# Kernel optimization log

Measured on AMD Instinct MI355X. Metric: run time of the kernel, lower is better.

## Reference

```python
import jax, jax.numpy as jnp
import numpy as np

B, S, D = 2, 11253, 256
NHEAD, NLEVEL, DFF = 8, 4, 1024
KERNEL = 2
NPOINT = KERNEL * KERNEL
HEAD_DIM = D // NHEAD
LEVEL_SHAPES = [(92, 92), (46, 46), (23, 23), (12, 12)]
LEVEL_STARTS = np.cumsum([0] + [h * w for h, w in LEVEL_SHAPES])[:-1]


def _kernel_indices():
    # BoxeR _create_kernel_indices: even kernel -> [-0.5, 0.5]/K, (x, y) order
    idx = np.arange(KERNEL, dtype=np.float32) - (KERNEL - 1) / 2.0
    i, j = np.meshgrid(idx, idx, indexing="ij")
    return jnp.asarray(np.stack([j, i], -1).reshape(-1, 2) / KERNEL)


KIDX = _kernel_indices()  # (NPOINT, 2) box-relative sample offsets


def layer_norm(x, w, b, eps=1e-5):
    mu = x.mean(-1, keepdims=True)
    var = ((x - mu) ** 2).mean(-1, keepdims=True)
    return (x - mu) * jax.lax.rsqrt(var + eps) * w + b


def setup_inputs() -> dict:
    key = jax.random.key(0)
    ks = jax.random.split(key, 12)

    def p(i, shape, scale=0.02):
        return jax.random.normal(ks[i], shape, jnp.float32) * scale

    cxcy = jax.random.uniform(ks[2], (B, S, 2), jnp.float32, minval=0.1, maxval=0.9)
    wh = jax.random.uniform(ks[3], (B, S, 2), jnp.float32, minval=0.02, maxval=0.2)
    return dict(
        src=jax.random.normal(ks[0], (B, S, D), jnp.float32),
        pos=jax.random.normal(ks[1], (B, S, D), jnp.float32),
        src_shape=jnp.asarray(np.array(LEVEL_SHAPES, np.int32)),
        src_mask=jnp.zeros((B, S), jnp.bool_),
        src_start_index=jnp.asarray(LEVEL_STARTS.astype(np.int32)),
        src_valid_ratios=jnp.ones((B, NLEVEL, 2), jnp.float32),
        ref_windows=jnp.concatenate([cxcy, wh], -1),
        value_w=p(4, (D, D)), value_b=jnp.zeros((D,), jnp.float32),
        out_w=p(5, (D, D)), out_b=jnp.zeros((D,), jnp.float32),
        box_w=p(6, (NHEAD * NLEVEL * 4, D)), box_b=jnp.zeros((NHEAD * NLEVEL * 4,), jnp.float32),
        attn_w=p(7, (NHEAD * NLEVEL * NPOINT, D)), attn_b=jnp.zeros((NHEAD * NLEVEL * NPOINT,), jnp.float32),
        lin1_w=p(8, (DFF, D)), lin1_b=jnp.zeros((DFF,), jnp.float32),
        lin2_w=p(9, (D, DFF)), lin2_b=jnp.zeros((D,), jnp.float32),
        norm1_w=jnp.ones((D,), jnp.float32), norm1_b=jnp.zeros((D,), jnp.float32),
        norm2_w=jnp.ones((D,), jnp.float32), norm2_b=jnp.zeros((D,), jnp.float32),
    )


def box_attention(q, src, src_mask, src_valid_ratios, ref_windows,
                  value_w, value_b, out_w, out_b, box_w, box_b, attn_w, attn_b):
    value = src @ value_w.T + value_b
    value = jnp.where(src_mask[..., None], 0.0, value)
    value = value.reshape(B, S, NHEAD, HEAD_DIM)

    # where-to-attend: per-head, per-level box offsets decoded around ref_windows (cx,cy,w,h)
    off = (q @ box_w.T + box_b).reshape(B, S, NHEAD, NLEVEL, 4)
    ref = ref_windows[:, :, None, None, :]
    boxes = ref + off / 8.0 * ref[..., jnp.array([2, 3, 2, 3])]
    center, size = boxes[..., None, :2], boxes[..., None, 2:]
    grid = center + KIDX * jax.nn.relu(size)  # (B,S,nh,L,P,2) in normalized [0,1] coords
    grid = grid * src_valid_ratios[:, None, None, :, None, :]

    attn = (q @ attn_w.T + attn_b).reshape(B, S, NHEAD, NLEVEL * NPOINT)
    attn = jax.nn.softmax(attn, -1).reshape(B, S, NHEAD, NLEVEL, NPOINT)

    out = jnp.zeros((B, NHEAD, S, HEAD_DIM), src.dtype)
    for lvl, (H, W) in enumerate(LEVEL_SHAPES):
        s0 = int(LEVEL_STARTS[lvl])
        v = jnp.transpose(value[:, s0:s0 + H * W], (0, 2, 1, 3))  # (B,nh,HW,hd)
        loc = jnp.transpose(grid[:, :, :, lvl], (0, 2, 1, 3, 4))  # (B,nh,S,P,2)
        # grid_sample bilinear, align_corners=False, zero padding
        px = loc[..., 0] * W - 0.5
        py = loc[..., 1] * H - 0.5
        x0, y0 = jnp.floor(px), jnp.floor(py)
        wx, wy = (px - x0)[..., None], (py - y0)[..., None]

        def gather(ix, iy):
            valid = (ix >= 0) & (ix < W) & (iy >= 0) & (iy < H)
            idx = (jnp.clip(iy, 0, H - 1) * W + jnp.clip(ix, 0, W - 1)).astype(jnp.int32)
            g = jnp.take_along_axis(v, idx.reshape(B, NHEAD, S * NPOINT)[..., None], axis=2)
            return g.reshape(B, NHEAD, S, NPOINT, HEAD_DIM) * valid[..., None]

        g00, g01 = gather(x0, y0), gather(x0 + 1, y0)
        g10, g11 = gather(x0, y0 + 1), gather(x0 + 1, y0 + 1)
        samp = (g00 * (1 - wx) + g01 * wx) * (1 - wy) + (g10 * (1 - wx) + g11 * wx) * wy
        aw = jnp.transpose(attn[:, :, :, lvl], (0, 2, 1, 3))  # (B,nh,S,P)
        out = out + jnp.einsum("bhspd,bhsp->bhsd", samp, aw)

    out = jnp.transpose(out, (0, 2, 1, 3)).reshape(B, S, D)
    return out @ out_w.T + out_b


def reference(src, pos, src_shape, src_mask, src_start_index, src_valid_ratios,
              ref_windows, value_w, value_b, out_w, out_b, box_w, box_b,
              attn_w, attn_b, lin1_w, lin1_b, lin2_w, lin2_b,
              norm1_w, norm1_b, norm2_w, norm2_b):
    # self-attn (box attention) + residual + LN
    src2 = box_attention(src + pos, src, src_mask, src_valid_ratios, ref_windows,
                         value_w, value_b, out_w, out_b, box_w, box_b, attn_w, attn_b)
    x = layer_norm(src + src2, norm1_w, norm1_b)
    # FFN + residual + LN (dropout=0 in eval)
    ff = jax.nn.relu(x @ lin1_w.T + lin1_b) @ lin2_w.T + lin2_b
    return layer_norm(x + ff, norm2_w, norm2_b)
```

## Files before the change

### kernel.cpp

```cpp
#include <hip/hip_runtime.h>
#include <hip/hip_bf16.h>
#include <hip/hip_fp16.h>

#define TOKENS 22506
#define SLEN   11253

typedef __bf16 bf16x8 __attribute__((ext_vector_type(8)));
typedef float  f32x4  __attribute__((ext_vector_type(4)));
typedef float  f32x2  __attribute__((ext_vector_type(2)));
typedef uint   u32x4  __attribute__((ext_vector_type(4)));

__device__ __forceinline__ ushort f2bu(float f) {
    __hip_bfloat16 h = __float2bfloat16(f);
    return *reinterpret_cast<ushort*>(&h);
}
__device__ __forceinline__ float bu2f(ushort u) {
    return __uint_as_float((uint)u << 16);
}
__device__ __forceinline__ uint pkf16(float a, float b) {
    __half2 h = __floats2half2_rn(a, b);
    return *reinterpret_cast<uint*>(&h);
}
__device__ __forceinline__ void gl16(const ushort* g, ushort* l) {
    __builtin_amdgcn_global_load_lds(
        (__attribute__((address_space(1))) void*)(g),
        (__attribute__((address_space(3))) void*)(l), 16, 0, 0);
}

template<bool RELU, bool NTSTORE>
__global__ __launch_bounds__(256) void gemm_small(
    const ushort* __restrict__ A0, const ushort* __restrict__ W0,
    const float* __restrict__ b0, ushort* __restrict__ C0,
    const ushort* __restrict__ A1, const ushort* __restrict__ W1,
    const float* __restrict__ b1, ushort* __restrict__ C1,
    int M, int N, int K)
{
    const bool zz = blockIdx.z != 0;
    const ushort* A   = zz ? A1 : A0;
    const ushort* W   = zz ? W1 : W0;
    const float* bias = zz ? b1 : b0;
    ushort* Cptr      = zz ? C1 : C0;

    __shared__ ushort smem[12288];
    const int tid  = threadIdx.x;
    const int lane = tid & 63;
    const int wid  = tid >> 6;
    const int wr = wid >> 1, wc = wid & 1;
    const int m0 = blockIdx.x * 64, n0 = blockIdx.y * 128;
    const int lrow = lane & 15, lhi = lane >> 4;

    const int arow = tid >> 2;
    const int scol = (tid & 3) << 3;
    const ushort* ga  = A + (size_t)min(m0 + arow, M - 1) * K + scol;
    const ushort* gb0 = W + (size_t)(n0 + arow)      * K + scol;
    const ushort* gb1 = W + (size_t)(n0 + arow + 64) * K + scol;

    f32x4 acc[2][4] = {};
    const int NT = K >> 5;

    gl16(ga,  &smem[tid * 8]);
    gl16(gb0, &smem[4096 + tid * 8]);
    gl16(gb1, &smem[4096 + tid * 8 + 2048]);

    int cur = 0;
    for (int t = 0; t < NT; ++t) {
        __syncthreads();
        if (t + 1 < NT) {
            const int k0 = (t + 1) << 5;
            const int nb = cur ^ 1;
            gl16(ga  + k0, &smem[nb * 2048 + tid * 8]);
            gl16(gb0 + k0, &smem[4096 + nb * 4096 + tid * 8]);
            gl16(gb1 + k0, &smem[4096 + nb * 4096 + tid * 8 + 2048]);
        }
        bf16x8 afr[2], bfr[4];
        #pragma unroll
        for (int m = 0; m < 2; ++m)
            afr[m] = *reinterpret_cast<const bf16x8*>(
                &smem[cur * 2048 + (wr * 32 + m * 16 + lrow) * 32 + lhi * 8]);
        #pragma unroll
        for (int n = 0; n < 4; ++n)
            bfr[n] = *reinterpret_cast<const bf16x8*>(
                &smem[4096 + cur * 4096 + (wc * 64 + n * 16 + lrow) * 32 + lhi * 8]);
        #pragma unroll
        for (int m = 0; m < 2; ++m)
            #pragma unroll
            for (int n = 0; n < 4; ++n)
                acc[m][n] = __builtin_amdgcn_mfma_f32_16x16x32_bf16(
                    afr[m], bfr[n], acc[m][n], 0, 0, 0);
        cur ^= 1;
    }

    __syncthreads();
    #pragma unroll
    for (int m = 0; m < 2; ++m) {
        #pragma unroll
        for (int n = 0; n < 4; ++n) {
            const int col = wc * 64 + n * 16 + lrow;
            const float bv = bias[n0 + col];
            #pragma unroll
            for (int r = 0; r < 4; ++r) {
                const int row = wr * 32 + m * 16 + lhi * 4 + r;
                float v = acc[m][n][r] + bv;
                if (RELU) v = fmaxf(v, 0.f);
                smem[row * 136 + col] = f2bu(v);
            }
        }
    }
    __syncthreads();
    #pragma unroll
    for (int i = 0; i < 4; ++i) {
        const int e = tid + i * 256;
        const int row = e >> 4, ch = e & 15;
        if (m0 + row < M) {
            const u32x4 v = *reinterpret_cast<const u32x4*>(&smem[row * 136 + ch * 8]);
            u32x4* dst = reinterpret_cast<u32x4*>(Cptr + (size_t)(m0 + row) * N + n0 + ch * 8);
            if (NTSTORE) __builtin_nontemporal_store(v, dst);
            else *dst = v;
        }
    }
}

__global__ __launch_bounds__(256) void prep_all(
    const float* __restrict__ vw, const float* __restrict__ bw,
    const float* __restrict__ aw, const float* __restrict__ ow,
    const float* __restrict__ l1, const float* __restrict__ l2,
    const float* __restrict__ bb, const float* __restrict__ ab,
    ushort* __restrict__ dstW, float* __restrict__ dstQB,
    const float4* __restrict__ src, const float4* __restrict__ pos,
    ushort4* __restrict__ srcb, ushort4* __restrict__ qb)
{
    const int blk = blockIdx.x;
    if (blk < 2817) {
        const int i = blk * 256 + threadIdx.x;
        if (i < 720896) {
            float v;
            if      (i <  65536) v = vw[i];
            else if (i <  98304) v = bw[i -  65536];
            else if (i < 131072) v = aw[i -  98304];
            else if (i < 196608) v = ow[i - 131072];
            else if (i < 458752) v = l1[i - 196608];
            else                 v = l2[i - 458752];
            dstW[i] = f2bu(v);
        } else if (i < 721152) {
            const int j = i - 720896;
            dstQB[j] = (j < 128) ? bb[j] : ab[j - 128];
        }
    } else {
        const int i = (blk - 2817) * 256 + threadIdx.x;
        if (i >= TOKENS * 64) return;
        const float4 s = src[i], p = pos[i];
        ushort4 us, uq;
        us.x = f2bu(s.x); us.y = f2bu(s.y); us.z = f2bu(s.z); us.w = f2bu(s.w);
        uq.x = f2bu(s.x + p.x); uq.y = f2bu(s.y + p.y);
        uq.z = f2bu(s.z + p.z); uq.w = f2bu(s.w + p.w);
        srcb[i] = us; qb[i] = uq;
    }
}

__global__ __launch_bounds__(256) void box_fused(
    const ushort* __restrict__ val,
    const ushort* __restrict__ qout,
    const float* __restrict__ refw,
    const float* __restrict__ vratio,
    ushort* __restrict__ attnout)
{
    __shared__ uint4 offs[64 * 17];
    __shared__ uint2 wts[64 * 17];
    const int tid = threadIdx.x;
    const int t0 = blockIdx.x * 8;

    {
        const int u = tid >> 2, lvl = tid & 3;
        const int t = min(t0 + (u >> 3), TOKENS - 1);
        const int h = u & 7;
        const int b = (t >= SLEN) ? 1 : 0;
        const ushort* qr = qout + (size_t)t * 256;

        const uint2 lu = *reinterpret_cast<const uint2*>(qr + 128 + h * 16 + lvl * 4);
        float e0 = __uint_as_float(lu.x << 16);
        float e1 = __uint_as_float(lu.x & 0xFFFF0000u);
        float e2 = __uint_as_float(lu.y << 16);
        float e3 = __uint_as_float(lu.y & 0xFFFF0000u);
        float mx = fmaxf(fmaxf(e0, e1), fmaxf(e2, e3));
        mx = fmaxf(mx, __shfl_xor(mx, 1));
        mx = fmaxf(mx, __shfl_xor(mx, 2));
        e0 = __expf(e0 - mx); e1 = __expf(e1 - mx);
        e2 = __expf(e2 - mx); e3 = __expf(e3 - mx);
        float ss = e0 + e1 + e2 + e3;
        ss += __shfl_xor(ss, 1);
        ss += __shfl_xor(ss, 2);
        const float inv = 1.f / ss;
        const float pe[4] = { e0 * inv, e1 * inv, e2 * inv, e3 * inv };

        const uint2 ou = *reinterpret_cast<const uint2*>(qr + h * 16 + lvl * 4);
        const float o0 = __uint_as_float(ou.x << 16) * 0.125f;
        const float o1 = __uint_as_float(ou.x & 0xFFFF0000u) * 0.125f;
        const float o2 = __uint_as_float(ou.y << 16) * 0.125f;
        const float o3 = __uint_as_float(ou.y & 0xFFFF0000u) * 0.125f;

        const float4 rw = *reinterpret_cast<const float4*>(refw + (size_t)t * 4);
        const int Ww = (lvl == 0) ? 92 : (lvl == 1) ? 46 : (lvl == 2) ? 23 : 12;
        const int s0 = (lvl == 0) ? 0 : (lvl == 1) ? 8464 : (lvl == 2) ? 10580 : 11109;
        const float vrx = vratio[(b * 4 + lvl) * 2 + 0];
        const float vry = vratio[(b * 4 + lvl) * 2 + 1];

        const float bx  = rw.x + o0 * rw.z;
        const float by  = rw.y + o1 * rw.w;
        const float bwd = fmaxf(rw.z + o2 * rw.z, 0.f);
        const float bhd = fmaxf(rw.w + o3 * rw.w, 0.f);

        #pragma unroll
        for (int k = 0; k < 4; ++k) {
            const float jx = (k & 1) ? 0.25f : -0.25f;
            const float iy = (k & 2) ? 0.25f : -0.25f;
            const float px = (bx + jx * bwd) * vrx * (float)Ww - 0.5f;
            const float py = (by + iy * bhd) * vry * (float)Ww - 0.5f;
            const float x0f = floorf(px), y0f = floorf(py);
            const int x0 = (int)x0f, y0 = (int)y0f;
            const float wx = px - x0f, wy = py - y0f;
            const float wp = pe[k];

            const bool vx0 = (x0 >= 0) && (x0 < Ww);
            const bool vx1 = (x0 + 1 >= 0) && (x0 + 1 < Ww);
            const bool vy0 = (y0 >= 0) && (y0 < Ww);
            const bool vy1 = (y0 + 1 >= 0) && (y0 + 1 < Ww);
            const int cx0 = min(max(x0, 0), Ww - 1);
            const int cx1 = min(max(x0 + 1, 0), Ww - 1);
            const int cy0 = min(max(y0, 0), Ww - 1);
            const int cy1 = min(max(y0 + 1, 0), Ww - 1);

            const float w00 = (vx0 && vy0) ? wp * (1.f - wx) * (1.f - wy) : 0.f;
            const float w01 = (vx1 && vy0) ? wp * wx         * (1.f - wy) : 0.f;
            const float w10 = (vx0 && vy1) ? wp * (1.f - wx) * wy         : 0.f;
            const float w11 = (vx1 && vy1) ? wp * wx         * wy         : 0.f;

            uint4 off4;
            off4.x = (uint)(s0 + cy0 * Ww + cx0) * 512u;
            off4.y = (uint)(s0 + cy0 * Ww + cx1) * 512u;
            off4.z = (uint)(s0 + cy1 * Ww + cx0) * 512u;
            off4.w = (uint)(s0 + cy1 * Ww + cx1) * 512u;

            const int p = lvl * 4 + k;
            offs[u * 17 + p] = off4;
            wts[u * 17 + p]  = make_uint2(pkf16(w00, w01), pkf16(w10, w11));
        }
    }
    __syncthreads();

    const int u = tid >> 2, dl = tid & 3;
    const int traw = t0 + (u >> 3);
    const int t = min(traw, TOKENS - 1);
    const int h = u & 7;
    const uint boff = (uint)(((t >= SLEN) ? SLEN * 512u : 0u) + h * 64u + dl * 16u);
    const char* base = (const char*)val;

    const uint4* po = &offs[u * 17];
    const uint2* pw = &wts[u * 17];
    f32x2 a0 = {0.f, 0.f}, a1 = {0.f, 0.f}, a2 = {0.f, 0.f}, a3 = {0.f, 0.f};

    #pragma unroll
    for (int g = 0; g < 8; ++g) {
        const uint4 oA = po[g * 2 + 0];
        const uint4 oB = po[g * 2 + 1];
        const uint2 wA = pw[g * 2 + 0];
        const uint2 wB = pw[g * 2 + 1];

        uint4 v0 = *reinterpret_cast<const uint4*>(base + (oA.x + boff));
        uint4 v1 = *reinterpret_cast<const uint4*>(base + (oA.y + boff));
        uint4 v2 = *reinterpret_cast<const uint4*>(base + (oA.z + boff));
        uint4 v3 = *reinterpret_cast<const uint4*>(base + (oA.w + boff));
        uint4 v4 = *reinterpret_cast<const uint4*>(base + (oB.x + boff));
        uint4 v5 = *reinterpret_cast<const uint4*>(base + (oB.y + boff));
        uint4 v6 = *reinterpret_cast<const uint4*>(base + (oB.w ^ oB.w ^ oB.z + boff));
        uint4 v7 = *reinterpret_cast<const uint4*>(base + (oB.w + boff));

        const float2 wAl = __half22float2(*reinterpret_cast<const __half2*>(&wA.x));
        const float2 wAh = __half22float2(*reinterpret_cast<const __half2*>(&wA.y));
        const float2 wBl = __half22float2(*reinterpret_cast<const __half2*>(&wB.x));
        const float2 wBh = __half22float2(*reinterpret_cast<const __half2*>(&wB.y));

        auto acc8 = [&](const uint4 v, const float w) {
            f32x2 wv; wv.x = w; wv.y = w;
            f32x2 tv;
            tv.x = __uint_as_float(v.x << 16);
            tv.y = __uint_as_float(v.x & 0xFFFF0000u);
            a0 += wv * tv;
            tv.x = __uint_as_float(v.y << 16);
            tv.y = __uint_as_float(v.y & 0xFFFF0000u);
            a1 += wv * tv;
            tv.x = __uint_as_float(v.z << 16);
            tv.y = __uint_as_float(v.z & 0xFFFF0000u);
            a2 += wv * tv;
            tv.x = __uint_as_float(v.w << 16);
            tv.y = __uint_as_float(v.w & 0xFFFF0000u);
            a3 += wv * tv;
        };
        acc8(v0, wAl.x); acc8(v1, wAl.y); acc8(v2, wAh.x); acc8(v3, wAh.y);
        acc8(v4, wBl.x); acc8(v5, wBl.y); acc8(v6, wBh.x); acc8(v7, wBh.y);
    }

    if (traw < TOKENS) {
        u32x4 o;
        o[0] = (uint)f2bu(a0.x) | ((uint)f2bu(a0.y) << 16);
        o[1] = (uint)f2bu(a1.x) | ((uint)f2bu(a1.y) << 16);
        o[2] = (uint)f2bu(a2.x) | ((uint)f2bu(a2.y) << 16);
        o[3] = (uint)f2bu(a3.x) | ((uint)f2bu(a3.y) << 16);
        *reinterpret_cast<u32x4*>(attnout + (size_t)t * 256 + h * 32 + dl * 8) = o;
    }
}

template<bool AF32, bool OUTF32>
__global__ __launch_bounds__(256) void ln_add2(
    const void* __restrict__ aptr, const ushort* __restrict__ bptr,
    const float* __restrict__ w, const float* __restrict__ bias,
    void* __restrict__ outp, int nrows)
{
    const int lane = threadIdx.x & 63, wv = threadIdx.x >> 6;
    const int row = blockIdx.x * 4 + wv;
    if (row >= nrows) return;
    const size_t base = (size_t)row * 256 + lane * 4;

    float4 av;
    if (AF32) {
        av = *reinterpret_cast<const float4*>((const float*)aptr + base);
    } else {
        const ushort4 u = *reinterpret_cast<const ushort4*>((const ushort*)aptr + base);
        av = make_float4(bu2f(u.x), bu2f(u.y), bu2f(u.z), bu2f(u.w));
    }
    const ushort4 ub = *reinterpret_cast<const ushort4*>(bptr + base);
    const float v0 = av.x + bu2f(ub.x), v1 = av.y + bu2f(ub.y);
    const float v2 = av.z + bu2f(ub.z), v3 = av.w + bu2f(ub.w);

    float s = v0 + v1 + v2 + v3;
    #pragma unroll
    for (int o = 32; o; o >>= 1) s += __shfl_xor(s, o);
    const float mu = s * (1.f / 256.f);
    const float d0 = v0 - mu, d1 = v1 - mu, d2 = v2 - mu, d3 = v3 - mu;
    float s2 = d0 * d0 + d1 * d1 + d2 * d2 + d3 * d3;
    #pragma unroll
    for (int o = 32; o; o >>= 1) s2 += __shfl_xor(s2, o);
    const float rs = rsqrtf(s2 * (1.f / 256.f) + 1e-5f);

    const float4 w4 = *reinterpret_cast<const float4*>(w + lane * 4);
    const float4 g4 = *reinterpret_cast<const float4*>(bias + lane * 4);
    const float r0 = d0 * rs * w4.x + g4.x;
    const float r1 = d1 * rs * w4.y + g4.y;
    const float r2 = d2 * rs * w4.z + g4.z;
    const float r3 = d3 * rs * w4.w + g4.w;
    if (OUTF32) {
        *reinterpret_cast<float4*>((float*)outp + base) = make_float4(r0, r1, r2, r3);
    } else {
        ushort4 u;
        u.x = f2bu(r0); u.y = f2bu(r1); u.z = f2bu(r2); u.w = f2bu(r3);
        *reinterpret_cast<ushort4*>((ushort*)outp + base) = u;
    }
}

extern "C" void kernel_launch(void* const* d_in, const int* in_sizes, int n_in,
                              void* d_out, int out_size, void* d_ws, size_t ws_size,
                              hipStream_t stream)
{
    const float* src     = (const float*)d_in[0];
    const float* pos     = (const float*)d_in[1];
    const float* vratio  = (const float*)d_in[5];
    const float* refw    = (const float*)d_in[6];
    const float* value_w = (const float*)d_in[7];
    const float* value_b = (const float*)d_in[8];
    const float* out_w   = (const float*)d_in[9];
    const float* out_b   = (const float*)d_in[10];
    const float* box_w   = (const float*)d_in[11];
    const float* box_b   = (const float*)d_in[12];
    const float* attn_w  = (const float*)d_in[13];
    const float* attn_b  = (const float*)d_in[14];
    const float* lin1_w  = (const float*)d_in[15];
    const float* lin1_b  = (const float*)d_in[16];
    const float* lin2_w  = (const float*)d_in[17];
    const float* lin2_b  = (const float*)d_in[18];
    const float* n1w     = (const float*)d_in[19];
    const float* n1b     = (const float*)d_in[20];
    const float* n2w     = (const float*)d_in[21];
    const float* n2b     = (const float*)d_in[22];

    char* wsb = (char*)d_ws;
    ushort* Wb    = (ushort*)(wsb);
    float*  qcb   = (float*)(wsb + 1441792);
    ushort* srcb  = (ushort*)(wsb + 1442816);
    ushort* qb    = (ushort*)(wsb + 12965888);
    ushort* valb  = (ushort*)(wsb + 24488960);
    ushort* qoutb = (ushort*)(wsb + 36012032);
    ushort* attb  = (ushort*)(wsb + 47535104);
    ushort* src2b = (ushort*)(wsb + 59058176);
    ushort* xbb   = (ushort*)(wsb + 70581248);
    ushort* hb    = (ushort*)(wsb + 82104320);
    ushort* yb    = (ushort*)(wsb + 128196608);

    const dim3 blk(256);

    prep_all<<<dim3(8444), blk, 0, stream>>>(
        value_w, box_w, attn_w, out_w, lin1_w, lin2_w, box_b, attn_b, Wb, qcb,
        (const float4*)src, (const float4*)pos, (ushort4*)srcb, (ushort4*)qb);

    gemm_small<false, false><<<dim3(352, 2, 2), blk, 0, stream>>>(
        srcb, Wb, value_b, valb,
        qb, Wb + 65536, qcb, qoutb, TOKENS, 256, 256);

    box_fused<<<dim3((TOKENS + 7) / 8), blk, 0, stream>>>(
        valb, qoutb, refw, vratio, attb);

    gemm_small<false, false><<<dim3(352, 2, 1), blk, 0, stream>>>(
        attb, Wb + 131072, out_b, src2b,
        attb, Wb + 131072, out_b, src2b, TOKENS, 256, 256);
    ln_add2<true, false><<<dim3((TOKENS + 3) / 4), blk, 0, stream>>>(
        src, src2b, n1w, n1b, xbb, TOKENS);
    gemm_small<true, true><<<dim3(352, 8, 1), blk, 0, stream>>>(
        xbb, Wb + 196608, lin1_b, hb,
        xbb, Wb + 196608, lin1_b, hb, TOKENS, 1024, 256);
    gemm_small<false, false><<<dim3(352, 2, 1), blk, 0, stream>>>(
        hb, Wb + 458752, lin2_b, yb,
        hb, Wb + 458752, lin2_b, yb, TOKENS, 256, 1024);
    ln_add2<false, true><<<dim3((TOKENS + 3) / 4), blk, 0, stream>>>(
        xbb, yb, n2w, n2b, (float*)d_out, TOKENS);
}
```

Baseline: 146.3 us.

## Store value projection as FP8 and gather FP8 in box attention

The value GEMM now writes its output as FP8 (e4m3) instead of bf16, and the box attention kernel gathers 8-byte FP8 chunks per lane and converts them with the hardware pk conversion builtins, or a software fallback when those are absent. Sample offsets in shared memory shrink from uint4 byte offsets to ushort4 token indices. This halves the gather traffic and the value buffer footprint in the memory-bound sampling stage. In exchange it loses value precision, which may push results past tolerance, and adds conversion ALU work.

```diff
diff --git a/kernel.cpp b/kernel.cpp
--- a/kernel.cpp
+++ b/kernel.cpp
@@ -10,6 +10,12 @@
 typedef float  f32x2  __attribute__((ext_vector_type(2)));
 typedef uint   u32x4  __attribute__((ext_vector_type(4)));
 
+#if defined(__has_builtin)
+#if __has_builtin(__builtin_amdgcn_cvt_pk_f32_fp8) && __has_builtin(__builtin_amdgcn_cvt_pk_fp8_f32)
+#define HAS_FP8CVT 1
+#endif
+#endif
+
 __device__ __forceinline__ ushort f2bu(float f) {
     __hip_bfloat16 h = __float2bfloat16(f);
     return *reinterpret_cast<ushort*>(&h);
@@ -27,19 +33,69 @@
         (__attribute__((address_space(3))) void*)(l), 16, 0, 0);
 }
 
-template<bool RELU, bool NTSTORE>
+#ifndef HAS_FP8CVT
+__device__ __forceinline__ uint enc_fp8(float x) {
+    if (!(fabsf(x) >= 0.f)) return 0;
+    uint u = __float_as_uint(x);
+    uint s = (u >> 24) & 0x80u;
+    float ax = fabsf(x);
+    if (ax >= 448.f) return s | 0x7Eu;
+    if (ax < 0.0009765625f) return s;
+    int e; frexpf(ax, &e);
+    int ue = e - 1;
+    if (ue < -6) {
+        int m = (int)(ax * 512.f + 0.5f);
+        if (m > 7) m = 7;
+        return s | (uint)m;
+    }
+    float q = ax * exp2f((float)(3 - ue));
+    int mi = (int)(q + 0.5f);
+    if (mi >= 16) { mi >>= 1; ++ue; if (ue > 8) return s | 0x7Eu; }
+    return s | ((uint)(ue + 7) << 3) | ((uint)mi & 7u);
+}
+__device__ __forceinline__ float dec_fp8(uint b) {
+    const float sgn = (b & 0x80u) ? -1.f : 1.f;
+    const uint e = (b >> 3) & 15u, m = b & 7u;
+    if (e == 0) return sgn * (float)m * 0.001953125f;
+    return sgn * (1.0f + (float)m * 0.125f) * exp2f((float)e - 7.f);
+}
+#endif
+
+__device__ __forceinline__ uint fp8pack4(float f0, float f1, float f2, float f3) {
+#ifdef HAS_FP8CVT
+    int p = 0;
+    p = __builtin_amdgcn_cvt_pk_fp8_f32(f0, f1, p, false);
+    p = __builtin_amdgcn_cvt_pk_fp8_f32(f2, f3, p, true);
+    return (uint)p;
+#else
+    return enc_fp8(f0) | (enc_fp8(f1) << 8) | (enc_fp8(f2) << 16) | (enc_fp8(f3) << 24);
+#endif
+}
+template<bool HI>
+__device__ __forceinline__ f32x2 fp8pair(uint w) {
+#ifdef HAS_FP8CVT
+    auto c = __builtin_amdgcn_cvt_pk_f32_fp8((int)w, HI);
+    f32x2 r; r.x = c[0]; r.y = c[1]; return r;
+#else
+    const uint sh = HI ? 16u : 0u;
+    f32x2 r; r.x = dec_fp8((w >> sh) & 0xFFu); r.y = dec_fp8((w >> (sh + 8)) & 0xFFu);
+    return r;
+#endif
+}
+
+template<bool RELU, bool NTSTORE, bool F8Z0>
 __global__ __launch_bounds__(256) void gemm_small(
     const ushort* __restrict__ A0, const ushort* __restrict__ W0,
-    const float* __restrict__ b0, ushort* __restrict__ C0,
+    const float* __restrict__ b0, void* __restrict__ C0,
     const ushort* __restrict__ A1, const ushort* __restrict__ W1,
-    const float* __restrict__ b1, ushort* __restrict__ C1,
+    const float* __restrict__ b1, void* __restrict__ C1,
     int M, int N, int K)
 {
     const bool zz = blockIdx.z != 0;
     const ushort* A   = zz ? A1 : A0;
     const ushort* W   = zz ? W1 : W0;
     const float* bias = zz ? b1 : b0;
-    ushort* Cptr      = zz ? C1 : C0;
+    void* Cptr        = zz ? C1 : C0;
 
     __shared__ ushort smem[12288];
     const int tid  = threadIdx.x;
@@ -107,15 +163,38 @@
         }
     }
     __syncthreads();
-    #pragma unroll
-    for (int i = 0; i < 4; ++i) {
-        const int e = tid + i * 256;
-        const int row = e >> 4, ch = e & 15;
-        if (m0 + row < M) {
-            const u32x4 v = *reinterpret_cast<const u32x4*>(&smem[row * 136 + ch * 8]);
-            u32x4* dst = reinterpret_cast<u32x4*>(Cptr + (size_t)(m0 + row) * N + n0 + ch * 8);
-            if (NTSTORE) __builtin_nontemporal_store(v, dst);
-            else *dst = v;
+    if (F8Z0 && !zz) {
+        #pragma unroll
+        for (int i = 0; i < 4; ++i) {
+            const int e = tid + i * 256;
+            const int row = e >> 4, ch = e & 15;
+            if (m0 + row < M) {
+                const u32x4 v = *reinterpret_cast<const u32x4*>(&smem[row * 136 + ch * 8]);
+                float f[8];
+                #pragma unroll
+                for (int j = 0; j < 4; ++j) {
+                    f[2 * j]     = __uint_as_float(v[j] << 16);
+                    f[2 * j + 1] = __uint_as_float(v[j] & 0xFFFF0000u);
+                }
+                uint2 o;
+                o.x = fp8pack4(f[0], f[1], f[2], f[3]);
+                o.y = fp8pack4(f[4], f[5], f[6], f[7]);
+                *reinterpret_cast<uint2*>(
+                    (unsigned char*)Cptr + (size_t)(m0 + row) * N + n0 + ch * 8) = o;
+            }
+        }
+    } else {
+        #pragma unroll
+        for (int i = 0; i < 4; ++i) {
+            const int e = tid + i * 256;
+            const int row = e >> 4, ch = e & 15;
+            if (m0 + row < M) {
+                const u32x4 v = *reinterpret_cast<const u32x4*>(&smem[row * 136 + ch * 8]);
+                u32x4* dst = reinterpret_cast<u32x4*>(
+                    (ushort*)Cptr + (size_t)(m0 + row) * N + n0 + ch * 8);
+                if (NTSTORE) __builtin_nontemporal_store(v, dst);
+                else *dst = v;
+            }
         }
     }
 }
@@ -158,13 +237,13 @@
 }
 
 __global__ __launch_bounds__(256) void box_fused(
-    const ushort* __restrict__ val,
+    const unsigned char* __restrict__ val,
     const ushort* __restrict__ qout,
     const float* __restrict__ refw,
     const float* __restrict__ vratio,
     ushort* __restrict__ attnout)
 {
-    __shared__ uint4 offs[64 * 17];
+    __shared__ ushort4 offs[64 * 17];
     __shared__ uint2 wts[64 * 17];
     const int tid = threadIdx.x;
     const int t0 = blockIdx.x * 8;
@@ -234,14 +313,14 @@
             const float w10 = (vx0 && vy1) ? wp * (1.f - wx) * wy         : 0.f;
             const float w11 = (vx1 && vy1) ? wp * wx         * wy         : 0.f;
 
-            uint4 off4;
-            off4.x = (uint)(s0 + cy0 * Ww + cx0) * 512u;
-            off4.y = (uint)(s0 + cy0 * Ww + cx1) * 512u;
-            off4.z = (uint)(s0 + cy1 * Ww + cx0) * 512u;
-            off4.w = (uint)(s0 + cy1 * Ww + cx1) * 512u;
+            ushort4 sp;
+            sp.x = (ushort)(s0 + cy0 * Ww + cx0);
+            sp.y = (ushort)(s0 + cy0 * Ww + cx1);
+            sp.z = (ushort)(s0 + cy1 * Ww + cx0);
+            sp.w = (ushort)(s0 + cy1 * Ww + cx1);
 
             const int p = lvl * 4 + k;
-            offs[u * 17 + p] = off4;
+            offs[u * 17 + p] = sp;
             wts[u * 17 + p]  = make_uint2(pkf16(w00, w01), pkf16(w10, w11));
         }
     }
@@ -251,52 +330,43 @@
     const int traw = t0 + (u >> 3);
     const int t = min(traw, TOKENS - 1);
     const int h = u & 7;
-    const uint boff = (uint)(((t >= SLEN) ? SLEN * 512u : 0u) + h * 64u + dl * 16u);
+    const uint boff = ((t >= SLEN) ? (uint)SLEN * 256u : 0u) + (uint)h * 32u + (uint)dl * 8u;
     const char* base = (const char*)val;
 
-    const uint4* po = &offs[u * 17];
+    const ushort4* po = &offs[u * 17];
     const uint2* pw = &wts[u * 17];
     f32x2 a0 = {0.f, 0.f}, a1 = {0.f, 0.f}, a2 = {0.f, 0.f}, a3 = {0.f, 0.f};
 
     #pragma unroll
     for (int g = 0; g < 8; ++g) {
-        const uint4 oA = po[g * 2 + 0];
-        const uint4 oB = po[g * 2 + 1];
+        const ushort4 sA = po[g * 2 + 0];
+        const ushort4 sB = po[g * 2 + 1];
         const uint2 wA = pw[g * 2 + 0];
         const uint2 wB = pw[g * 2 + 1];
 
-        uint4 v0 = *reinterpret_cast<const uint4*>(base + (oA.x + boff));
-        uint4 v1 = *reinterpret_cast<const uint4*>(base + (oA.y + boff));
-        uint4 v2 = *reinterpret_cast<const uint4*>(base + (oA.z + boff));
-        uint4 v3 = *reinterpret_cast<const uint4*>(base + (oA.w + boff));
-        uint4 v4 = *reinterpret_cast<const uint4*>(base + (oB.x + boff));
-        uint4 v5 = *reinterpret_cast<const uint4*>(base + (oB.y + boff));
-        uint4 v6 = *reinterpret_cast<const uint4*>(base + (oB.w ^ oB.w ^ oB.z + boff));
-        uint4 v7 = *reinterpret_cast<const uint4*>(base + (oB.w + boff));
+        const uint2 v0 = *reinterpret_cast<const uint2*>(base + (((uint)sA.x << 8) + boff));
+        const uint2 v1 = *reinterpret_cast<const uint2*>(base + (((uint)sA.y << 8) + boff));
+        const uint2 v2 = *reinterpret_cast<const uint2*>(base + (((uint)sA.z << 8) + boff));
+        const uint2 v3 = *reinterpret_cast<const uint2*>(base + (((uint)sA.w << 8) + boff));
+        const uint2 v4 = *reinterpret_cast<const uint2*>(base + (((uint)sB.x << 8) + boff));
+        const uint2 v5 = *reinterpret_cast<const uint2*>(base + (((uint)sB.y << 8) + boff));
+        const uint2 v6 = *reinterpret_cast<const uint2*>(base + (((uint)sB.z << 8) + boff));
+        const uint2 v7 = *reinterpret_cast<const uint2*>(base + (((uint)sB.w << 8) + boff));
 
         const float2 wAl = __half22float2(*reinterpret_cast<const __half2*>(&wA.x));
         const float2 wAh = __half22float2(*reinterpret_cast<const __half2*>(&wA.y));
         const float2 wBl = __half22float2(*reinterpret_cast<const __half2*>(&wB.x));
         const float2 wBh = __half22float2(*reinterpret_cast<const __half2*>(&wB.y));
 
-        auto acc8 = [&](const uint4 v, const float w) {
+        auto accf8 = [&](const uint2 v, const float w) {
             f32x2 wv; wv.x = w; wv.y = w;
-            f32x2 tv;
-            tv.x = __uint_as_float(v.x << 16);
-            tv.y = __uint_as_float(v.x & 0xFFFF0000u);
-            a0 += wv * tv;
-            tv.x = __uint_as_float(v.y << 16);
-            tv.y = __uint_as_float(v.y & 0xFFFF0000u);
-            a1 += wv * tv;
-            tv.x = __uint_as_float(v.z << 16);
-            tv.y = __uint_as_float(v.z & 0xFFFF0000u);
-            a2 += wv * tv;
-            tv.x = __uint_as_float(v.w << 16);
-            tv.y = __uint_as_float(v.w & 0xFFFF0000u);
-            a3 += wv * tv;
+            a0 += wv * fp8pair<false>(v.x);
+            a1 += wv * fp8pair<true>(v.x);
+            a2 += wv * fp8pair<false>(v.y);
+            a3 += wv * fp8pair<true>(v.y);
         };
-        acc8(v0, wAl.x); acc8(v1, wAl.y); acc8(v2, wAh.x); acc8(v3, wAh.y);
-        acc8(v4, wBl.x); acc8(v5, wBl.y); acc8(v6, wBh.x); acc8(v7, wBh.y);
+        accf8(v0, wAl.x); accf8(v1, wAl.y); accf8(v2, wAh.x); accf8(v3, wAh.y);
+        accf8(v4, wBl.x); accf8(v5, wBl.y); accf8(v6, wBh.x); accf8(v7, wBh.y);
     }
 
     if (traw < TOKENS) {
@@ -386,7 +456,7 @@
     float*  qcb   = (float*)(wsb + 1441792);
     ushort* srcb  = (ushort*)(wsb + 1442816);
     ushort* qb    = (ushort*)(wsb + 12965888);
-    ushort* valb  = (ushort*)(wsb + 24488960);
+    unsigned char* valb = (unsigned char*)(wsb + 24488960);
     ushort* qoutb = (ushort*)(wsb + 36012032);
     ushort* attb  = (ushort*)(wsb + 47535104);
     ushort* src2b = (ushort*)(wsb + 59058176);
@@ -400,22 +470,22 @@
         value_w, box_w, attn_w, out_w, lin1_w, lin2_w, box_b, attn_b, Wb, qcb,
         (const float4*)src, (const float4*)pos, (ushort4*)srcb, (ushort4*)qb);
 
-    gemm_small<false, false><<<dim3(352, 2, 2), blk, 0, stream>>>(
+    gemm_small<false, false, true><<<dim3(352, 2, 2), blk, 0, stream>>>(
         srcb, Wb, value_b, valb,
         qb, Wb + 65536, qcb, qoutb, TOKENS, 256, 256);
 
     box_fused<<<dim3((TOKENS + 7) / 8), blk, 0, stream>>>(
         valb, qoutb, refw, vratio, attb);
 
-    gemm_small<false, false><<<dim3(352, 2, 1), blk, 0, stream>>>(
+    gemm_small<false, false, false><<<dim3(352, 2, 1), blk, 0, stream>>>(
         attb, Wb + 131072, out_b, src2b,
         attb, Wb + 131072, out_b, src2b, TOKENS, 256, 256);
     ln_add2<true, false><<<dim3((TOKENS + 3) / 4), blk, 0, stream>>>(
         src, src2b, n1w, n1b, xbb, TOKENS);
-    gemm_small<true, true><<<dim3(352, 8, 1), blk, 0, stream>>>(
+    gemm_small<true, true, false><<<dim3(352, 8, 1), blk, 0, stream>>>(
         xbb, Wb + 196608, lin1_b, hb,
         xbb, Wb + 196608, lin1_b, hb, TOKENS, 1024, 256);
-    gemm_small<false, false><<<dim3(352, 2, 1), blk, 0, stream>>>(
+    gemm_small<false, false, false><<<dim3(352, 2, 1), blk, 0, stream>>>(
         hb, Wb + 458752, lin2_b, yb,
         hb, Wb + 458752, lin2_b, yb, TOKENS, 256, 1024);
     ln_add2<false, true><<<dim3((TOKENS + 3) / 4), blk, 0, stream>>>(
```

After: 134.9 us. 7.7% less time.
